# Optimization experiments

Measured on AMD Instinct MI355X. Metric: run time of the kernel, lower is better.

The kernel has to match this reference:

```python
import jax, jax.numpy as jnp
import numpy as np
from jax import lax

HEADS = 8
DIM_HEAD = 64
INNER = HEADS * DIM_HEAD  # 512
LOG_SCALE_MAX = float(np.log(100.0))  # clamp for clamp_exp (SwinV2-style max temperature 1/0.01)
EPS_NORM = 1e-12  # F.normalize eps
EPS_LN = 1e-5


def setup_inputs() -> dict:
    key = jax.random.key(0)
    ks = jax.random.split(key, 6)
    b, c, h, w = 2, 256, 48, 48
    x = jax.random.normal(ks[0], (b, c, h, w), jnp.float32)
    w_in = jax.random.normal(ks[1], (3 * INNER, c), jnp.float32) * (c ** -0.5)
    b_in = jnp.zeros((3 * INNER,), jnp.float32)
    # learnable log-scale, init log(d_head ** -0.5), per head
    softmax_scale = jnp.full((HEADS, 1, 1), float(np.log(DIM_HEAD ** -0.5)), jnp.float32)
    w_dw = jax.random.normal(ks[2], (INNER, 1, 3, 3), jnp.float32) * (1.0 / 3.0)
    w_pw = jax.random.normal(ks[3], (2 * c, INNER), jnp.float32) * (INNER ** -0.5)
    gamma = jnp.full((2 * c,), 1e-3, jnp.float32)  # norm init_weight=0.001
    beta = jnp.zeros((2 * c,), jnp.float32)
    return {"x": x, "w_in": w_in, "b_in": b_in, "softmax_scale": softmax_scale,
            "w_dw": w_dw, "w_pw": w_pw, "gamma": gamma, "beta": beta}


def _l2norm(t):
    n = jnp.sqrt(jnp.sum(t * t, axis=-1, keepdims=True))
    return t / jnp.maximum(n, EPS_NORM)


def reference(x, w_in, b_in, softmax_scale, w_dw, w_pw, gamma, beta):
    b, c, h, w = x.shape
    s = h * w
    # proj_in: 1x1 conv then 'b (h c) x y -> b h x y c'
    y = jnp.einsum('bchw,oc->bohw', x, w_in) + b_in[None, :, None, None]
    y = y.reshape(b, HEADS, 3 * DIM_HEAD, h, w).transpose(0, 1, 3, 4, 2)  # b H x y (3*dh)
    y = y.reshape(b, HEADS, s, 3 * DIM_HEAD)
    q, k, v = jnp.split(y, 3, axis=-1)  # each [b, H, s, dh]
    # scaled cosine attention
    qn, kn = _l2norm(q), _l2norm(k)
    scale = jnp.exp(jnp.minimum(softmax_scale, LOG_SCALE_MAX))  # clamp_exp, [H,1,1]
    sim = jnp.einsum('bhid,bhjd->bhij', qn, kn) * scale[None]
    attn = jax.nn.softmax(sim, axis=-1)
    out = jnp.einsum('bhij,bhjd->bhid', attn, v)  # [b,H,s,dh]
    # unsplit heads -> 'b (h w) c' -> 'b c h w'
    update = out.transpose(0, 2, 1, 3).reshape(b, s, INNER)
    update = update.transpose(0, 2, 1).reshape(b, INNER, h, w)
    # proj_out: depthwise 3x3 (no bias) + pointwise 1x1 (no bias)
    dw = lax.conv_general_dilated(update, w_dw, (1, 1), 'SAME',
                                  feature_group_count=INNER,
                                  dimension_numbers=('NCHW', 'OIHW', 'NCHW'))
    pw = jnp.einsum('bchw,oc->bohw', dw, w_pw)  # [b, 2c, h, w]
    # channelwise layernorm with small init weight (norm_scales_and_shifts)
    mu = jnp.mean(pw, axis=1, keepdims=True)
    var = jnp.var(pw, axis=1, keepdims=True)
    normed = (pw - mu) * lax.rsqrt(var + EPS_LN)
    normed = normed * gamma[None, :, None, None] + beta[None, :, None, None]
    scales, shifts = jnp.split(normed, 2, axis=1)  # each [b, c, h, w]
    return shifts + x * scales
```

## Files before the change

kernel.cpp:

```cpp
#include <hip/hip_runtime.h>

#define B_ 2
#define C_ 256
#define S_ 2304
#define DH_ 64
#define O3_ 1536
#define INNER_ 512
#define LOGSMAX 4.605170185988092f
#define LOG2E 1.4426950408889634f

typedef __attribute__((ext_vector_type(8))) short short8;
typedef __attribute__((ext_vector_type(4))) float f32x4;
typedef __attribute__((ext_vector_type(16))) float f32x16;
typedef __attribute__((ext_vector_type(4))) unsigned short us4;
typedef __attribute__((ext_vector_type(2))) unsigned u32x2;
typedef __attribute__((ext_vector_type(4))) unsigned u32x4;
typedef __bf16 bf16x8 __attribute__((ext_vector_type(8)));

__device__ __forceinline__ unsigned short f2bf(float f) {
  unsigned u = __builtin_bit_cast(unsigned, f);
  u += 0x7FFFu + ((u >> 16) & 1u);
  return (unsigned short)(u >> 16);
}
__device__ __forceinline__ float bf2f(unsigned short h) {
  return __builtin_bit_cast(float, (unsigned)h << 16);
}
__device__ __forceinline__ bf16x8 as_bf(short8 v) {
  return __builtin_bit_cast(bf16x8, v);
}
__device__ __forceinline__ float fexp2(float x) {
#if __has_builtin(__builtin_amdgcn_exp2f)
  return __builtin_amdgcn_exp2f(x);
#else
  return __expf(x * 0.6931471805599453f);
#endif
}
__device__ __forceinline__ float frcp(float x) {
#if __has_builtin(__builtin_amdgcn_rcpf)
  return __builtin_amdgcn_rcpf(x);
#else
  return 1.f / x;
#endif
}
__device__ __forceinline__ unsigned pack_hi16(unsigned b, unsigned a) {
  return __builtin_amdgcn_perm(b, a, 0x07060302u);
}
__device__ __forceinline__ unsigned pack_lo16(unsigned b, unsigned a) {
  return __builtin_amdgcn_perm(b, a, 0x05040100u);
}
__device__ __forceinline__ unsigned pk2(float a, float b) {
  unsigned ua = __builtin_bit_cast(unsigned, a) + 0x8000u;
  unsigned ub = __builtin_bit_cast(unsigned, b) + 0x8000u;
  return pack_hi16(ub, ua);
}

__global__ __launch_bounds__(256) void k_prep(const float* __restrict__ x,
                                              const float* __restrict__ w_in,
                                              const float* __restrict__ w_pw,
                                              unsigned short* __restrict__ xT,
                                              unsigned short* __restrict__ w_inb,
                                              unsigned short* __restrict__ w_pwb) {
  __shared__ float tile[64][65];
  int blk = blockIdx.x;
  int t = threadIdx.x;
  if (blk < 288) {
    int p0 = (blk % 36) * 64, c0 = ((blk / 36) % 4) * 64, b = blk / 144;
    const float* xb = x + (size_t)b * C_ * S_;
#pragma unroll
    for (int i = 0; i < 16; i++) {
      int c = i * 4 + (t >> 6);
      int p = t & 63;
      tile[c][p] = xb[(size_t)(c0 + c) * S_ + p0 + p];
    }
    __syncthreads();
    unsigned short* xTb = xT + (size_t)b * S_ * C_;
#pragma unroll
    for (int i = 0; i < 16; i++) {
      int p = i * 4 + (t >> 6);
      int c = t & 63;
      xTb[(size_t)(p0 + p) * C_ + c0 + c] = f2bf(tile[c][p]);
    }
  } else if (blk < 288 + 1536) {
    int i = (blk - 288) * 256 + t;
    w_inb[i] = f2bf(w_in[i]);
  } else {
    int i = (blk - 1824) * 256 + t;
    w_pwb[i] = f2bf(w_pw[i]);
  }
}

__global__ __launch_bounds__(256) void k_gemm_qkv(const unsigned short* __restrict__ A,
                                                  const unsigned short* __restrict__ BT,
                                                  const float* __restrict__ b_in,
                                                  const float* __restrict__ ss,
                                                  unsigned char* __restrict__ qn,
                                                  unsigned char* __restrict__ kn,
                                                  unsigned short* __restrict__ vv) {
  __shared__ __align__(16) unsigned short As[64][72];
  __shared__ __align__(16) unsigned short Bs[128][72];
  int t = threadIdx.x;
  int lane = t & 63, wv = t >> 6;
  int quad = lane >> 4, r15 = lane & 15;
  int by = blockIdx.y;
  int m0 = by * 64, n0 = blockIdx.x * 128;
  int b = blockIdx.z;
  const unsigned short* BTb = BT + (size_t)b * S_ * C_;

  f32x4 acc[4][2] = {};

  int srA = t >> 2, scA = (t & 3) * 16;
  int srB = t >> 1, scB = (t & 1) * 32;
  const unsigned short* ag = A + (size_t)(m0 + srA) * C_ + scA;
  const unsigned short* bg = BTb + (size_t)(n0 + srB) * C_ + scB;

  for (int k0 = 0; k0 < C_; k0 += 64) {
    short8 a0 = *(const short8*)(ag + k0);
    short8 a1 = *(const short8*)(ag + k0 + 8);
    short8 b0 = *(const short8*)(bg + k0);
    short8 b1 = *(const short8*)(bg + k0 + 8);
    short8 b2 = *(const short8*)(bg + k0 + 16);
    short8 b3 = *(const short8*)(bg + k0 + 24);
    __syncthreads();
    *(short8*)&As[srA][scA] = a0;
    *(short8*)&As[srA][scA + 8] = a1;
    *(short8*)&Bs[srB][scB] = b0;
    *(short8*)&Bs[srB][scB + 8] = b1;
    *(short8*)&Bs[srB][scB + 16] = b2;
    *(short8*)&Bs[srB][scB + 24] = b3;
    __syncthreads();
#pragma unroll
    for (int ks = 0; ks < 2; ks++) {
      short8 af[4], bfr[2];
#pragma unroll
      for (int i = 0; i < 4; i++) af[i] = *(const short8*)&As[i * 16 + r15][ks * 32 + quad * 8];
#pragma unroll
      for (int j = 0; j < 2; j++) bfr[j] = *(const short8*)&Bs[wv * 32 + j * 16 + r15][ks * 32 + quad * 8];
#pragma unroll
      for (int i = 0; i < 4; i++)
#pragma unroll
        for (int j = 0; j < 2; j++)
          acc[i][j] = __builtin_amdgcn_mfma_f32_16x16x32_bf16(as_bf(af[i]), as_bf(bfr[j]), acc[i][j], 0, 0, 0);
    }
  }

  int h = by / 3, seg = by - h * 3;
  int bh = b * 8 + h;
  f32x4 bi[4];
#pragma unroll
  for (int i = 0; i < 4; i++) bi[i] = *(const f32x4*)&b_in[m0 + i * 16 + quad * 4];
  float bv[4][2][4];
  float ssq0 = 0.f, ssq1 = 0.f;
#pragma unroll
  for (int i = 0; i < 4; i++)
#pragma unroll
    for (int rr = 0; rr < 4; rr++) {
      float v0 = acc[i][0][rr] + bi[i][rr];
      float v1 = acc[i][1][rr] + bi[i][rr];
      bv[i][0][rr] = v0;
      bv[i][1][rr] = v1;
      ssq0 += v0 * v0;
      ssq1 += v1 * v1;
    }
  if (seg < 2) {
    float sc = (seg == 0) ? __expf(fminf(ss[h], LOGSMAX)) * LOG2E : 1.f;
    ssq0 += __shfl_xor(ssq0, 16);
    ssq0 += __shfl_xor(ssq0, 32);
    ssq1 += __shfl_xor(ssq1, 16);
    ssq1 += __shfl_xor(ssq1, 32);
    float inv0 = sc / fmaxf(sqrtf(ssq0), 1e-12f);
    float inv1 = sc / fmaxf(sqrtf(ssq1), 1e-12f);
    unsigned char* dst = (seg == 0 ? qn : kn) + (size_t)bh * S_ * DH_;
#pragma unroll
    for (int i = 0; i < 4; i++)
#pragma unroll
      for (int j = 0; j < 2; j++) {
        float iv = j ? inv1 : inv0;
        int pk = __builtin_amdgcn_cvt_pk_fp8_f32(bv[i][j][0] * iv, bv[i][j][1] * iv, 0, false);
        pk = __builtin_amdgcn_cvt_pk_fp8_f32(bv[i][j][2] * iv, bv[i][j][3] * iv, pk, true);
        int p = n0 + wv * 32 + j * 16 + r15;
        *(int*)&dst[(size_t)p * DH_ + i * 16 + quad * 4] = pk;
      }
  } else {
    unsigned short* dst = vv + (size_t)bh * S_ * DH_;
#pragma unroll
    for (int i = 0; i < 4; i++)
#pragma unroll
      for (int j = 0; j < 2; j++) {
        us4 o = {f2bf(bv[i][j][0]), f2bf(bv[i][j][1]), f2bf(bv[i][j][2]), f2bf(bv[i][j][3])};
        int p = n0 + wv * 32 + j * 16 + r15;
        *(us4*)&dst[(size_t)p * DH_ + i * 16 + quad * 4] = o;
      }
  }
}

__global__ __launch_bounds__(128) void k_gemm2(const unsigned short* __restrict__ A,
                                               const unsigned short* __restrict__ BT,
                                               float* __restrict__ outp,
                                               int M, int N, int K) {
  __shared__ __align__(16) unsigned short As[64][72];
  __shared__ __align__(16) unsigned short Bs[64][72];
  int t = threadIdx.x;
  int lane = t & 63, wv = t >> 6;
  int quad = lane >> 4, r15 = lane & 15;
  int m0 = blockIdx.y * 64, n0 = blockIdx.x * 64;
  int b = blockIdx.z;
  const unsigned short* BTb = BT + (size_t)b * N * K;

  f32x4 acc[4][2] = {};

  int sr = t >> 1, sc = (t & 1) * 32;
  const unsigned short* ag = A + (size_t)(m0 + sr) * K + sc;
  const unsigned short* bg = BTb + (size_t)(n0 + sr) * K + sc;

  for (int k0 = 0; k0 < K; k0 += 64) {
    short8 a0 = *(const short8*)(ag + k0);
    short8 a1 = *(const short8*)(ag + k0 + 8);
    short8 a2 = *(const short8*)(ag + k0 + 16);
    short8 a3 = *(const short8*)(ag + k0 + 24);
    short8 b0 = *(const short8*)(bg + k0);
    short8 b1 = *(const short8*)(bg + k0 + 8);
    short8 b2 = *(const short8*)(bg + k0 + 16);
    short8 b3 = *(const short8*)(bg + k0 + 24);
    __syncthreads();
    *(short8*)&As[sr][sc] = a0;
    *(short8*)&As[sr][sc + 8] = a1;
    *(short8*)&As[sr][sc + 16] = a2;
    *(short8*)&As[sr][sc + 24] = a3;
    *(short8*)&Bs[sr][sc] = b0;
    *(short8*)&Bs[sr][sc + 8] = b1;
    *(short8*)&Bs[sr][sc + 16] = b2;
    *(short8*)&Bs[sr][sc + 24] = b3;
    __syncthreads();
#pragma unroll
    for (int ks = 0; ks < 2; ks++) {
      short8 af[4], bfr[2];
#pragma unroll
      for (int i = 0; i < 4; i++) af[i] = *(const short8*)&As[i * 16 + r15][ks * 32 + quad * 8];
#pragma unroll
      for (int j = 0; j < 2; j++) bfr[j] = *(const short8*)&Bs[wv * 32 + j * 16 + r15][ks * 32 + quad * 8];
#pragma unroll
      for (int i = 0; i < 4; i++)
#pragma unroll
        for (int j = 0; j < 2; j++)
          acc[i][j] = __builtin_amdgcn_mfma_f32_16x16x32_bf16(as_bf(af[i]), as_bf(bfr[j]), acc[i][j], 0, 0, 0);
    }
  }
  float* Cb = outp + (size_t)b * M * N;
#pragma unroll
  for (int i = 0; i < 4; i++)
#pragma unroll
    for (int j = 0; j < 2; j++)
#pragma unroll
      for (int rr = 0; rr < 4; rr++) {
        int row = m0 + i * 16 + quad * 4 + rr;
        int col = n0 + wv * 32 + j * 16 + r15;
        Cb[(size_t)row * N + col] = acc[i][j][rr];
      }
}

__global__ __launch_bounds__(256) void k_attn(const unsigned char* __restrict__ qn,
                                              const unsigned char* __restrict__ kn,
                                              const unsigned short* __restrict__ vv,
                                              const float* __restrict__ ss,
                                              unsigned short* __restrict__ attnp,
                                              float* __restrict__ lp) {
  __shared__ __align__(16) unsigned char Ks[64][72];
  __shared__ __align__(16) unsigned short Vs[64][72];
  int t = threadIdx.x;
  int w = t >> 6;
  int lane = t & 63;
  int l31 = lane & 31, hi = lane >> 5;
  int bh = blockIdx.x;
  int q0 = blockIdx.y * 128 + w * 32;
  int split = blockIdx.z;
  int ktbase = split * 9;
  const unsigned char* qb = qn + (size_t)bh * S_ * DH_;
  const unsigned char* kb = kn + (size_t)bh * S_ * DH_;
  const unsigned short* vb = vv + (size_t)bh * S_ * DH_;
  float shift2 = __expf(fminf(ss[bh & 7], LOGSMAX)) * LOG2E;

  const unsigned char* qrow = qb + (size_t)(q0 + l31) * DH_ + hi * 8;
  long qf[4];
#pragma unroll
  for (int ks = 0; ks < 4; ks++) qf[ks] = *(const long*)(qrow + ks * 16);

  const f32x16 z16 = {};
  f32x16 O0 = z16, O1 = z16;
  float l_part = 0.f;

  int srow = t >> 2;
  int scol = (t & 3) * 16;
  const unsigned char* kg = kb + ((size_t)(ktbase * 64) + srow) * DH_ + scol;

  int dp = w * 8 + ((t & 63) >> 3);
  int koct = t & 7;
  const unsigned* vg32 = (const unsigned*)vb + ((size_t)(ktbase * 64 + koct * 8)) * 32 + dp;

  uint4 kr = *(const uint4*)kg;
  unsigned lv[8];
#pragma unroll
  for (int kk = 0; kk < 8; kk++) lv[kk] = vg32[(size_t)kk * 32];

  for (int i = 0; i < 9; i++) {
    __syncthreads();
    *(uint4*)&Ks[srow][scol] = kr;
    {
      u32x4 ev = {pack_lo16(lv[1], lv[0]), pack_lo16(lv[3], lv[2]),
                  pack_lo16(lv[5], lv[4]), pack_lo16(lv[7], lv[6])};
      u32x4 od = {pack_hi16(lv[1], lv[0]), pack_hi16(lv[3], lv[2]),
                  pack_hi16(lv[5], lv[4]), pack_hi16(lv[7], lv[6])};
      *(u32x4*)&Vs[2 * dp][koct * 8] = ev;
      *(u32x4*)&Vs[2 * dp + 1][koct * 8] = od;
    }
    __syncthreads();
    if (i < 8) {
      kr = *(const uint4*)(kg + (size_t)(i + 1) * 64 * DH_);
      const unsigned* vg = vg32 + (size_t)(i + 1) * 64 * 32;
#pragma unroll
      for (int kk = 0; kk < 8; kk++) lv[kk] = vg[(size_t)kk * 32];
    }
    f32x16 sc0, sc1;
    {
      long a0 = *(const long*)&Ks[l31][hi * 8];
      long a1 = *(const long*)&Ks[32 + l31][hi * 8];
      sc0 = __builtin_amdgcn_mfma_f32_32x32x16_fp8_fp8(a0, qf[0], z16, 0, 0, 0);
      sc1 = __builtin_amdgcn_mfma_f32_32x32x16_fp8_fp8(a1, qf[0], z16, 0, 0, 0);
    }
#pragma unroll
    for (int ks = 1; ks < 4; ks++) {
      long a0 = *(const long*)&Ks[l31][ks * 16 + hi * 8];
      long a1 = *(const long*)&Ks[32 + l31][ks * 16 + hi * 8];
      sc0 = __builtin_amdgcn_mfma_f32_32x32x16_fp8_fp8(a0, qf[ks], sc0, 0, 0, 0);
      sc1 = __builtin_amdgcn_mfma_f32_32x32x16_fp8_fp8(a1, qf[ks], sc1, 0, 0, 0);
    }
#pragma unroll
    for (int mt = 0; mt < 2; mt++) {
      const f32x16& s = mt ? sc1 : sc0;
      unsigned pk[8];
      float lsum = 0.f;
#pragma unroll
      for (int g2 = 0; g2 < 4; g2++) {
        float e0 = fexp2(s[g2 * 4 + 0] - shift2);
        float e1 = fexp2(s[g2 * 4 + 1] - shift2);
        float e2 = fexp2(s[g2 * 4 + 2] - shift2);
        float e3 = fexp2(s[g2 * 4 + 3] - shift2);
        lsum += (e0 + e1) + (e2 + e3);
        pk[2 * g2] = pk2(e0, e1);
        pk[2 * g2 + 1] = pk2(e2, e3);
      }
      l_part += lsum;
#pragma unroll
      for (int half = 0; half < 2; half++) {
        int gb = half * 4;
        unsigned ya = hi ? pk[gb + 0] : pk[gb + 2];
        unsigned yb = hi ? pk[gb + 1] : pk[gb + 3];
        unsigned ra = __shfl_xor(ya, 32);
        unsigned rb = __shfl_xor(yb, 32);
        u32x4 fd;
        fd[0] = hi ? ra : pk[gb + 0];
        fd[1] = hi ? rb : pk[gb + 1];
        fd[2] = hi ? pk[gb + 2] : ra;
        fd[3] = hi ? pk[gb + 3] : rb;
        short8 pb = __builtin_bit_cast(short8, fd);
        int ks = mt * 2 + half;
        short8 va0 = *(const short8*)&Vs[l31][ks * 16 + hi * 8];
        short8 va1 = *(const short8*)&Vs[32 + l31][ks * 16 + hi * 8];
        O0 = __builtin_amdgcn_mfma_f32_32x32x16_bf16(as_bf(va0), as_bf(pb), O0, 0, 0, 0);
        O1 = __builtin_amdgcn_mfma_f32_32x32x16_bf16(as_bf(va1), as_bf(pb), O1, 0, 0, 0);
      }
    }
  }
  float l = l_part + __shfl_xor(l_part, 32);
  if (hi == 0) lp[((size_t)(split * 16 + bh)) * S_ + q0 + l31] = l;
  unsigned short* orow = attnp + (((size_t)(split * 16 + bh)) * S_ + q0 + l31) * DH_;
#pragma unroll
  for (int mt = 0; mt < 2; mt++) {
    const f32x16& O = mt ? O1 : O0;
#pragma unroll
    for (int g = 0; g < 4; g++) {
      us4 o4 = {f2bf(O[g * 4 + 0]), f2bf(O[g * 4 + 1]), f2bf(O[g * 4 + 2]), f2bf(O[g * 4 + 3])};
      *(us4*)&orow[mt * 32 + g * 8 + hi * 4] = o4;
    }
  }
}

__global__ __launch_bounds__(256) void k_dwconv(const unsigned short* __restrict__ attnp,
                                                const float* __restrict__ lp,
                                                const float* __restrict__ w_dw,
                                                unsigned short* __restrict__ dwb) {
  int t = threadIdx.x;
  int d = t & 63;
  int pj = t >> 6;
  int p = blockIdx.y * 4 + pj;
  int bh = blockIdx.x;
  int b = bh >> 3, h = bh & 7;
  int yy = p / 48, xx = p % 48;
  const unsigned short* a0 = attnp + (size_t)bh * S_ * DH_ + d;
  const unsigned short* a1 = attnp + ((size_t)(16 + bh)) * S_ * DH_ + d;
  const unsigned short* a2 = attnp + ((size_t)(32 + bh)) * S_ * DH_ + d;
  const unsigned short* a3 = attnp + ((size_t)(48 + bh)) * S_ * DH_ + d;
  const float* l0 = lp + (size_t)bh * S_;
  const float* l1 = lp + (size_t)(16 + bh) * S_;
  const float* l2 = lp + (size_t)(32 + bh) * S_;
  const float* l3 = lp + (size_t)(48 + bh) * S_;
  int ch = h * 64 + d;
  float w[9];
#pragma unroll
  for (int i = 0; i < 9; i++) w[i] = w_dw[ch * 9 + i];
  float acc = 0.f;
#pragma unroll
  for (int dy = -1; dy <= 1; dy++) {
    int y2 = yy + dy;
    if (y2 < 0 || y2 >= 48) continue;
#pragma unroll
    for (int dx = -1; dx <= 1; dx++) {
      int x2 = xx + dx;
      if (x2 < 0 || x2 >= 48) continue;
      int p2 = y2 * 48 + x2;
      float rl = frcp(l0[p2] + l1[p2] + l2[p2] + l3[p2]);
      float v = (bf2f(a0[(size_t)p2 * DH_]) + bf2f(a1[(size_t)p2 * DH_]) +
                 bf2f(a2[(size_t)p2 * DH_]) + bf2f(a3[(size_t)p2 * DH_])) * rl;
      acc += v * w[(dy + 1) * 3 + dx + 1];
    }
  }
  dwb[((size_t)b * S_ + p) * INNER_ + ch] = f2bf(acc);
}

__global__ __launch_bounds__(256) void k_ln_final(const float* __restrict__ pw,
                                                  const float* __restrict__ gamma,
                                                  const float* __restrict__ beta,
                                                  const float* __restrict__ x,
                                                  float* __restrict__ out) {
  __shared__ float s_s0[32][8], s_s1[32][8], s_q0[32][8], s_q1[32][8];
  int t = threadIdx.x;
  int pl = t & 7, g = t >> 3;
  int b = blockIdx.y;
  int p = blockIdx.x * 16 + pl * 2;
  const float* pwb = pw + (size_t)b * INNER_ * S_ + p;
  float s0 = 0.f, s1 = 0.f, q0 = 0.f, q1 = 0.f;
#pragma unroll
  for (int j = 0; j < 16; j++) {
    float2 v = *(const float2*)&pwb[(size_t)(g * 16 + j) * S_];
    s0 += v.x; s1 += v.y;
    q0 += v.x * v.x; q1 += v.y * v.y;
  }
  s_s0[g][pl] = s0; s_s1[g][pl] = s1;
  s_q0[g][pl] = q0; s_q1[g][pl] = q1;
  __syncthreads();
  float t0 = 0.f, t1 = 0.f, u0 = 0.f, u1 = 0.f;
#pragma unroll
  for (int i = 0; i < 32; i++) {
    t0 += s_s0[i][pl]; t1 += s_s1[i][pl];
    u0 += s_q0[i][pl]; u1 += s_q1[i][pl];
  }
  float mu0 = t0 * (1.f / 512.f), mu1 = t1 * (1.f / 512.f);
  float rs0 = rsqrtf(u0 * (1.f / 512.f) - mu0 * mu0 + 1e-5f);
  float rs1 = rsqrtf(u1 * (1.f / 512.f) - mu1 * mu1 + 1e-5f);
  const float* xb = x + (size_t)b * C_ * S_ + p;
  float* ob = out + (size_t)b * C_ * S_ + p;
#pragma unroll
  for (int j = 0; j < 8; j++) {
    int cc = g * 8 + j;
    float ga = gamma[cc], be = beta[cc];
    float gs = gamma[cc + 256], bs = beta[cc + 256];
    float2 pv = *(const float2*)&pwb[(size_t)cc * S_];
    float2 sv = *(const float2*)&pwb[(size_t)(cc + 256) * S_];
    float2 xv = *(const float2*)&xb[(size_t)cc * S_];
    float sc0 = (pv.x - mu0) * rs0 * ga + be;
    float sc1 = (pv.y - mu1) * rs1 * ga + be;
    float sh0 = (sv.x - mu0) * rs0 * gs + bs;
    float sh1 = (sv.y - mu1) * rs1 * gs + bs;
    float2 o;
    o.x = sh0 + xv.x * sc0;
    o.y = sh1 + xv.y * sc1;
    *(float2*)&ob[(size_t)cc * S_] = o;
  }
}

extern "C" void kernel_launch(void* const* d_in, const int* in_sizes, int n_in,
                              void* d_out, int out_size, void* d_ws, size_t ws_size,
                              hipStream_t stream) {
  const float* x = (const float*)d_in[0];
  const float* w_in = (const float*)d_in[1];
  const float* b_in = (const float*)d_in[2];
  const float* ss = (const float*)d_in[3];
  const float* w_dw = (const float*)d_in[4];
  const float* w_pw = (const float*)d_in[5];
  const float* gamma = (const float*)d_in[6];
  const float* beta = (const float*)d_in[7];
  float* out = (float*)d_out;
  char* ws = (char*)d_ws;

  unsigned short* xT = (unsigned short*)(ws + 0);
  unsigned short* w_inb = (unsigned short*)(ws + 2359296);
  unsigned short* w_pwb = (unsigned short*)(ws + 3145728);
  unsigned char* qn = (unsigned char*)(ws + 3670016);
  unsigned char* kn = (unsigned char*)(ws + 6029312);
  unsigned short* vv = (unsigned short*)(ws + 8388608);
  unsigned short* dwb = (unsigned short*)(ws + 13107200);
  float* lp = (float*)(ws + 17825792);
  unsigned short* attnp = (unsigned short*)(ws + 18415616);
  float* pw = (float*)(ws + 37289984);

  k_prep<<<2848, 256, 0, stream>>>(x, w_in, w_pw, xT, w_inb, w_pwb);
  k_gemm_qkv<<<dim3(18, 24, 2), 256, 0, stream>>>(w_inb, xT, b_in, ss, qn, kn, vv);
  k_attn<<<dim3(16, 18, 4), 256, 0, stream>>>(qn, kn, vv, ss, attnp, lp);
  k_dwconv<<<dim3(16, 576), 256, 0, stream>>>(attnp, lp, w_dw, dwb);
  k_gemm2<<<dim3(36, 8, 2), 128, 0, stream>>>(w_pwb, dwb, pw, INNER_, S_, INNER_);
  k_ln_final<<<dim3(144, 2), 256, 0, stream>>>(pw, gamma, beta, x, out);
}
```

Baseline: 166.6 us.

## Store V transposed for attention and write pointwise output as bf16

The QKV GEMM now writes V in a transposed [d][s] layout, so the attention kernel loads V tiles with straight 16-byte vector loads and stores them to shared memory directly, with no perm-based repacking. The QKV store for V becomes scattered 2-byte writes. Separately, the pointwise GEMM writes its output in bf16 instead of fp32, roughly halving the traffic into the layernorm kernel. The cost is lower precision in the layernorm statistics and narrow, poorly coalesced writes in the producer kernels.

```diff
diff --git a/kernel.cpp b/kernel.cpp
--- a/kernel.cpp
+++ b/kernel.cpp
@@ -44,9 +44,6 @@
 }
 __device__ __forceinline__ unsigned pack_hi16(unsigned b, unsigned a) {
   return __builtin_amdgcn_perm(b, a, 0x07060302u);
-}
-__device__ __forceinline__ unsigned pack_lo16(unsigned b, unsigned a) {
-  return __builtin_amdgcn_perm(b, a, 0x05040100u);
 }
 __device__ __forceinline__ unsigned pk2(float a, float b) {
   unsigned ua = __builtin_bit_cast(unsigned, a) + 0x8000u;
@@ -95,7 +92,7 @@
                                                   const float* __restrict__ ss,
                                                   unsigned char* __restrict__ qn,
                                                   unsigned char* __restrict__ kn,
-                                                  unsigned short* __restrict__ vv) {
+                                                  unsigned short* __restrict__ vT) {
   __shared__ __align__(16) unsigned short As[64][72];
   __shared__ __align__(16) unsigned short Bs[128][72];
   int t = threadIdx.x;
@@ -181,21 +178,24 @@
         *(int*)&dst[(size_t)p * DH_ + i * 16 + quad * 4] = pk;
       }
   } else {
-    unsigned short* dst = vv + (size_t)bh * S_ * DH_;
+    unsigned short* dst = vT + (size_t)bh * DH_ * S_;
 #pragma unroll
     for (int i = 0; i < 4; i++)
 #pragma unroll
       for (int j = 0; j < 2; j++) {
-        us4 o = {f2bf(bv[i][j][0]), f2bf(bv[i][j][1]), f2bf(bv[i][j][2]), f2bf(bv[i][j][3])};
         int p = n0 + wv * 32 + j * 16 + r15;
-        *(us4*)&dst[(size_t)p * DH_ + i * 16 + quad * 4] = o;
+#pragma unroll
+        for (int rr = 0; rr < 4; rr++) {
+          int d = i * 16 + quad * 4 + rr;
+          dst[(size_t)d * S_ + p] = f2bf(bv[i][j][rr]);
+        }
       }
   }
 }
 
 __global__ __launch_bounds__(128) void k_gemm2(const unsigned short* __restrict__ A,
                                                const unsigned short* __restrict__ BT,
-                                               float* __restrict__ outp,
+                                               unsigned short* __restrict__ outp,
                                                int M, int N, int K) {
   __shared__ __align__(16) unsigned short As[64][72];
   __shared__ __align__(16) unsigned short Bs[64][72];
@@ -245,7 +245,7 @@
           acc[i][j] = __builtin_amdgcn_mfma_f32_16x16x32_bf16(as_bf(af[i]), as_bf(bfr[j]), acc[i][j], 0, 0, 0);
     }
   }
-  float* Cb = outp + (size_t)b * M * N;
+  unsigned short* Cb = outp + (size_t)b * M * N;
 #pragma unroll
   for (int i = 0; i < 4; i++)
 #pragma unroll
@@ -254,13 +254,13 @@
       for (int rr = 0; rr < 4; rr++) {
         int row = m0 + i * 16 + quad * 4 + rr;
         int col = n0 + wv * 32 + j * 16 + r15;
-        Cb[(size_t)row * N + col] = acc[i][j][rr];
+        Cb[(size_t)row * N + col] = f2bf(acc[i][j][rr]);
       }
 }
 
 __global__ __launch_bounds__(256) void k_attn(const unsigned char* __restrict__ qn,
                                               const unsigned char* __restrict__ kn,
-                                              const unsigned short* __restrict__ vv,
+                                              const unsigned short* __restrict__ vT,
                                               const float* __restrict__ ss,
                                               unsigned short* __restrict__ attnp,
                                               float* __restrict__ lp) {
@@ -276,7 +276,7 @@
   int ktbase = split * 9;
   const unsigned char* qb = qn + (size_t)bh * S_ * DH_;
   const unsigned char* kb = kn + (size_t)bh * S_ * DH_;
-  const unsigned short* vb = vv + (size_t)bh * S_ * DH_;
+  const unsigned short* vb = vT + (size_t)bh * DH_ * S_;
   float shift2 = __expf(fminf(ss[bh & 7], LOGSMAX)) * LOG2E;
 
   const unsigned char* qrow = qb + (size_t)(q0 + l31) * DH_ + hi * 8;
@@ -289,35 +289,25 @@
   float l_part = 0.f;
 
   int srow = t >> 2;
-  int scol = (t & 3) * 16;
-  const unsigned char* kg = kb + ((size_t)(ktbase * 64) + srow) * DH_ + scol;
-
-  int dp = w * 8 + ((t & 63) >> 3);
-  int koct = t & 7;
-  const unsigned* vg32 = (const unsigned*)vb + ((size_t)(ktbase * 64 + koct * 8)) * 32 + dp;
+  int scolK = (t & 3) * 16;
+  int scolV = (t & 3) * 16;
+  const unsigned char* kg = kb + ((size_t)(ktbase * 64) + srow) * DH_ + scolK;
+  const unsigned short* vg = vb + (size_t)srow * S_ + ktbase * 64 + scolV;
 
   uint4 kr = *(const uint4*)kg;
-  unsigned lv[8];
-#pragma unroll
-  for (int kk = 0; kk < 8; kk++) lv[kk] = vg32[(size_t)kk * 32];
+  short8 vr0 = *(const short8*)vg;
+  short8 vr1 = *(const short8*)(vg + 8);
 
   for (int i = 0; i < 9; i++) {
     __syncthreads();
-    *(uint4*)&Ks[srow][scol] = kr;
-    {
-      u32x4 ev = {pack_lo16(lv[1], lv[0]), pack_lo16(lv[3], lv[2]),
-                  pack_lo16(lv[5], lv[4]), pack_lo16(lv[7], lv[6])};
-      u32x4 od = {pack_hi16(lv[1], lv[0]), pack_hi16(lv[3], lv[2]),
-                  pack_hi16(lv[5], lv[4]), pack_hi16(lv[7], lv[6])};
-      *(u32x4*)&Vs[2 * dp][koct * 8] = ev;
-      *(u32x4*)&Vs[2 * dp + 1][koct * 8] = od;
-    }
+    *(uint4*)&Ks[srow][scolK] = kr;
+    *(short8*)&Vs[srow][scolV] = vr0;
+    *(short8*)&Vs[srow][scolV + 8] = vr1;
     __syncthreads();
     if (i < 8) {
       kr = *(const uint4*)(kg + (size_t)(i + 1) * 64 * DH_);
-      const unsigned* vg = vg32 + (size_t)(i + 1) * 64 * 32;
-#pragma unroll
-      for (int kk = 0; kk < 8; kk++) lv[kk] = vg[(size_t)kk * 32];
+      vr0 = *(const short8*)(vg + (i + 1) * 64);
+      vr1 = *(const short8*)(vg + (i + 1) * 64 + 8);
     }
     f32x16 sc0, sc1;
     {
@@ -426,7 +416,7 @@
   dwb[((size_t)b * S_ + p) * INNER_ + ch] = f2bf(acc);
 }
 
-__global__ __launch_bounds__(256) void k_ln_final(const float* __restrict__ pw,
+__global__ __launch_bounds__(256) void k_ln_final(const unsigned short* __restrict__ pw,
                                                   const float* __restrict__ gamma,
                                                   const float* __restrict__ beta,
                                                   const float* __restrict__ x,
@@ -436,13 +426,15 @@
   int pl = t & 7, g = t >> 3;
   int b = blockIdx.y;
   int p = blockIdx.x * 16 + pl * 2;
-  const float* pwb = pw + (size_t)b * INNER_ * S_ + p;
+  const unsigned short* pwb = pw + (size_t)b * INNER_ * S_ + p;
   float s0 = 0.f, s1 = 0.f, q0 = 0.f, q1 = 0.f;
 #pragma unroll
   for (int j = 0; j < 16; j++) {
-    float2 v = *(const float2*)&pwb[(size_t)(g * 16 + j) * S_];
-    s0 += v.x; s1 += v.y;
-    q0 += v.x * v.x; q1 += v.y * v.y;
+    unsigned u = *(const unsigned*)&pwb[(size_t)(g * 16 + j) * S_];
+    float vx = bf2f((unsigned short)(u & 0xffffu));
+    float vy = bf2f((unsigned short)(u >> 16));
+    s0 += vx; s1 += vy;
+    q0 += vx * vx; q1 += vy * vy;
   }
   s_s0[g][pl] = s0; s_s1[g][pl] = s1;
   s_q0[g][pl] = q0; s_q1[g][pl] = q1;
@@ -463,13 +455,17 @@
     int cc = g * 8 + j;
     float ga = gamma[cc], be = beta[cc];
     float gs = gamma[cc + 256], bs = beta[cc + 256];
-    float2 pv = *(const float2*)&pwb[(size_t)cc * S_];
-    float2 sv = *(const float2*)&pwb[(size_t)(cc + 256) * S_];
+    unsigned pu = *(const unsigned*)&pwb[(size_t)cc * S_];
+    unsigned su = *(const unsigned*)&pwb[(size_t)(cc + 256) * S_];
     float2 xv = *(const float2*)&xb[(size_t)cc * S_];
-    float sc0 = (pv.x - mu0) * rs0 * ga + be;
-    float sc1 = (pv.y - mu1) * rs1 * ga + be;
-    float sh0 = (sv.x - mu0) * rs0 * gs + bs;
-    float sh1 = (sv.y - mu1) * rs1 * gs + bs;
+    float pv0 = bf2f((unsigned short)(pu & 0xffffu));
+    float pv1 = bf2f((unsigned short)(pu >> 16));
+    float sv0 = bf2f((unsigned short)(su & 0xffffu));
+    float sv1 = bf2f((unsigned short)(su >> 16));
+    float sc0 = (pv0 - mu0) * rs0 * ga + be;
+    float sc1 = (pv1 - mu1) * rs1 * ga + be;
+    float sh0 = (sv0 - mu0) * rs0 * gs + bs;
+    float sh1 = (sv1 - mu1) * rs1 * gs + bs;
     float2 o;
     o.x = sh0 + xv.x * sc0;
     o.y = sh1 + xv.y * sc1;
@@ -496,15 +492,15 @@
   unsigned short* w_pwb = (unsigned short*)(ws + 3145728);
   unsigned char* qn = (unsigned char*)(ws + 3670016);
   unsigned char* kn = (unsigned char*)(ws + 6029312);
-  unsigned short* vv = (unsigned short*)(ws + 8388608);
+  unsigned short* vT = (unsigned short*)(ws + 8388608);
   unsigned short* dwb = (unsigned short*)(ws + 13107200);
   float* lp = (float*)(ws + 17825792);
   unsigned short* attnp = (unsigned short*)(ws + 18415616);
-  float* pw = (float*)(ws + 37289984);
+  unsigned short* pw = (unsigned short*)(ws + 37289984);
 
   k_prep<<<2848, 256, 0, stream>>>(x, w_in, w_pw, xT, w_inb, w_pwb);
-  k_gemm_qkv<<<dim3(18, 24, 2), 256, 0, stream>>>(w_inb, xT, b_in, ss, qn, kn, vv);
-  k_attn<<<dim3(16, 18, 4), 256, 0, stream>>>(qn, kn, vv, ss, attnp, lp);
+  k_gemm_qkv<<<dim3(18, 24, 2), 256, 0, stream>>>(w_inb, xT, b_in, ss, qn, kn, vT);
+  k_attn<<<dim3(16, 18, 4), 256, 0, stream>>>(qn, kn, vT, ss, attnp, lp);
   k_dwconv<<<dim3(16, 576), 256, 0, stream>>>(attnp, lp, w_dw, dwb);
   k_gemm2<<<dim3(36, 8, 2), 128, 0, stream>>>(w_pwb, dwb, pw, INNER_, S_, INNER_);
   k_ln_final<<<dim3(144, 2), 256, 0, stream>>>(pw, gamma, beta, x, out);
```

Result: faster. 160.9 us (-3.5%).
